# Kernel optimization log

Hardware: AMD Instinct MI355X
Metric: run time of the kernel (lower is better)

Reference implementation:

```python
import jax, jax.numpy as jnp
import numpy as np

# Dims: B=32 batch, C=64 feat channels, Np=192 priors, No=72 row offsets,
# Ns=36 pooled sample points (maxpool kernel 2), Hd=64 fc hidden.
B, C, Np, No, Hd = 32, 64, 192, 72, 64
NS_POOL = 2  # n_offsets // sample_points
REG_DIM = No + 4  # reg_layers output


def bilinear_sample(feat, gx, gy):
    """torch F.grid_sample(align_corners=True) equivalent for in-range coords.
    feat: [B,C,H,W]; gx,gy: [B,Np,S] normalized to [-1,1]. -> [B,C,Np,S]."""
    Bb, Cc, H, W = feat.shape
    ix = (gx + 1.0) * 0.5 * (W - 1)
    iy = (gy + 1.0) * 0.5 * (H - 1)
    ix0f = jnp.floor(ix); iy0f = jnp.floor(iy)
    wx = ix - ix0f; wy = iy - iy0f
    ix0 = jnp.clip(ix0f.astype(jnp.int32), 0, W - 1)
    iy0 = jnp.clip(iy0f.astype(jnp.int32), 0, H - 1)
    ix1 = jnp.clip(ix0 + 1, 0, W - 1)
    iy1 = jnp.clip(iy0 + 1, 0, H - 1)
    ff = feat.reshape(Bb, Cc, H * W)
    S = gx.shape[1] * gx.shape[2]
    def gather(iy_, ix_):
        idx = (iy_ * W + ix_).reshape(Bb, 1, S)
        g = jnp.take_along_axis(ff, jnp.broadcast_to(idx, (Bb, Cc, S)), axis=2)
        return g.reshape(Bb, Cc, gx.shape[1], gx.shape[2])
    v00 = gather(iy0, ix0); v01 = gather(iy0, ix1)
    v10 = gather(iy1, ix0); v11 = gather(iy1, ix1)
    wx = wx[:, None]; wy = wy[:, None]  # broadcast over C
    return (v00 * (1 - wx) * (1 - wy) + v01 * wx * (1 - wy)
            + v10 * (1 - wx) * wy + v11 * wx * wy)


def _mlp2(h, Ws, bs):
    # two stacked Linear+ReLU layers (num_fc=2)
    for i in range(2):
        h = jax.nn.relu(h @ Ws[i] + bs[i])
    return h


def setup_inputs() -> dict:
    key = jax.random.key(0)
    ks = jax.random.split(key, 24)
    w = lambda k, sh: jax.random.normal(k, sh, dtype=jnp.float32) * 0.05
    return {
        "x0": jax.random.normal(ks[0], (B, C, 40, 100), dtype=jnp.float32),
        "x1": jax.random.normal(ks[1], (B, C, 20, 50), dtype=jnp.float32),
        "x2": jax.random.normal(ks[2], (B, C, 10, 25), dtype=jnp.float32),
        "prior_xs0": jax.random.uniform(ks[3], (Np, No), dtype=jnp.float32),
        "l_weight": w(ks[4], (No,)),              # self.l embedding, sigmoid gate
        "lsgi_w": w(ks[5], (3, C, C)),            # per-stage lsgi projection
        "fc_w": w(ks[6], (C, Hd)), "fc_b": w(ks[7], (Hd,)),
        "cls_w": w(ks[8], (2, Hd, Hd)), "cls_b": w(ks[9], (2, Hd)),
        "cls_ow": w(ks[10], (Hd, 2)), "cls_ob": w(ks[11], (2,)),
        "reg_w": w(ks[12], (2, Hd, Hd)), "reg_b": w(ks[13], (2, Hd)),
        "reg_ow": w(ks[14], (Hd, REG_DIM)), "reg_ob": w(ks[15], (REG_DIM,)),
        "loc_w": w(ks[16], (2, Hd, Hd)), "loc_b": w(ks[17], (2, Hd)),
        "loc_ow": w(ks[18], (Hd, 1)), "loc_ob": w(ks[19], (1,)),
    }


def reference(x0, x1, x2, prior_xs0, l_weight, lsgi_w, fc_w, fc_b,
              cls_w, cls_b, cls_ow, cls_ob, reg_w, reg_b, reg_ow, reg_ob,
              loc_w, loc_b, loc_ow, loc_ob):
    pyramid = [x2, x1, x0]  # reversed: coarsest level first (stage 0)
    prior_feat_ys = jnp.linspace(1.0, 0.0, No, dtype=jnp.float32)
    gy = jnp.broadcast_to((prior_feat_ys * 2.0 - 1.0)[None, None, :], (B, Np, No))
    prior_xs = jnp.broadcast_to(prior_xs0[None], (B, Np, No))
    gate = jax.nn.sigmoid(l_weight)[:, None]  # [No,1]
    stage_feats = []
    outs = []
    for s in range(3):
        gx = prior_xs * 2.0 - 1.0
        pooled = bilinear_sample(pyramid[s], gx, gy)          # [B,C,Np,No]
        pooled = jnp.transpose(pooled, (0, 2, 3, 1)) * gate   # [B,Np,No,C]
        pooled = jax.nn.relu(jnp.einsum('bnoc,cd->bnod', pooled, lsgi_w[s]))
        # MaxPool2d kernel (2,1) over the offset axis -> Ns=36 sample points
        comp = pooled.reshape(B, Np, No // NS_POOL, NS_POOL, C).max(axis=3)
        stage_feats.append(comp)
        # cross-stage fusion (global head): mean over stages and sample points
        fused = jnp.stack(stage_feats, 0).mean(axis=0).mean(axis=2)  # [B,Np,C]
        fc = jax.nn.relu(fused @ fc_w + fc_b)                        # [B,Np,Hd]
        cls = _mlp2(fc, cls_w, cls_b) @ cls_ow + cls_ob              # [B,Np,2]
        reg = _mlp2(fc, reg_w, reg_b) @ reg_ow + reg_ob              # [B,Np,No+4]
        loc = _mlp2(fc, loc_w, loc_b) @ loc_ow + loc_ob              # [B,Np,1]
        outs.append(jnp.concatenate([cls, reg, loc], axis=-1))      # [B,Np,79]
        # refine anchors for next stage from predicted xs
        prior_xs = jax.nn.sigmoid(reg[..., 4:])
    return jnp.stack(outs, axis=0)  # [3,B,Np,79]
```

## Files before the change

### kernel.cpp

```cpp
#include <hip/hip_runtime.h>
#include <hip/hip_bf16.h>

#define Bq   32
#define Cq   64
#define NPq  192
#define NOq  72
#define PTS  (NPq * NOq)
#define REGD 76
#define OUTD 79

typedef __attribute__((ext_vector_type(8))) short short8;
typedef __attribute__((ext_vector_type(4))) float float4v;

__device__ inline unsigned short f2bf(float x) {
    __hip_bfloat16 h = __float2bfloat16(x);
    return *reinterpret_cast<unsigned short*>(&h);
}
__device__ inline float bf2f(unsigned short u) {
    unsigned int x = ((unsigned int)u) << 16;
    float f;
    __builtin_memcpy(&f, &x, 4);
    return f;
}

__global__ __launch_bounds__(256) void build_tables_kernel(
    const float* __restrict__ f0,
    const float* __restrict__ f1,
    const float* __restrict__ f2,
    const float* __restrict__ lw,
    unsigned short* __restrict__ t0,
    unsigned short* __restrict__ t1,
    unsigned short* __restrict__ t2)
{
    __shared__ float sRow[64 * 101];

    const int tid = threadIdx.x;
    const int o   = blockIdx.x / 96;
    const int sb  = blockIdx.x - o * 96;
    const int s   = sb >> 5;
    const int b   = sb & 31;

    const float* feat; unsigned short* tab; int H, W;
    if (s == 0)      { feat = f0; tab = t0; H = 10; W = 25; }
    else if (s == 1) { feat = f1; tab = t1; H = 20; W = 50; }
    else             { feat = f2; tab = t2; H = 40; W = 100; }
    const int Wp = W + 1;

    const float ys = 1.0f - (float)o * (1.0f / 71.0f);
    const float iy = ys * (float)(H - 1);
    const float fy = floorf(iy);
    const float wy = iy - fy;
    int iy0 = (int)fy; iy0 = iy0 < 0 ? 0 : (iy0 > H - 1 ? H - 1 : iy0);
    const int iy1 = (iy0 + 1 > H - 1) ? H - 1 : iy0 + 1;
    const float gate = 1.0f / (1.0f + __expf(-lw[o]));

    const float* fb = feat + (size_t)b * 64 * H * W;
    const int iy0W = iy0 * W, iy1W = iy1 * W;

    const int tot = 64 * W;
    for (int idx = tid; idx < tot; idx += 256) {
        const int c = idx / W;
        const int x = idx - c * W;
        const float* f = fb + c * (H * W);
        sRow[c * Wp + x] = ((1.0f - wy) * f[iy0W + x] + wy * f[iy1W + x]) * gate;
    }
    __syncthreads();

    unsigned short* to = tab + (size_t)(b * NOq + o) * Wp * 64;
    const int tot2 = Wp * 64;
    for (int idx = tid; idx < tot2; idx += 256) {
        const int x = idx >> 6;
        const int c = idx & 63;
        const int xx = (x < W) ? x : (W - 1);
        to[idx] = f2bf(sRow[c * Wp + xx]);
    }
}

template<int W>
__global__ __launch_bounds__(256) void fused_pool_head_kernel(
    const unsigned short* __restrict__ tab,
    const float* __restrict__ xsrc, const int xstride,
    const float* __restrict__ lsgi,
    float* __restrict__ sumFeat,
    const int stage,
    const float* __restrict__ fc_w,  const float* __restrict__ fc_b,
    const float* __restrict__ cls_w, const float* __restrict__ cls_b,
    const float* __restrict__ cls_ow, const float* __restrict__ cls_ob,
    const float* __restrict__ reg_w, const float* __restrict__ reg_b,
    const float* __restrict__ reg_ow, const float* __restrict__ reg_ob,
    const float* __restrict__ loc_w, const float* __restrict__ loc_b,
    const float* __restrict__ loc_ow, const float* __restrict__ loc_ob,
    float* __restrict__ out, float* __restrict__ xs_next)
{
    constexpr int Wp = W + 1;
    __shared__ __align__(16) float sF [8][68];
    __shared__ __align__(16) float sC [8][68];
    __shared__ __align__(16) float sT1[8][68];
    __shared__ __align__(16) float sT2[8][68];
    __shared__ __align__(16) float sWt[4864];

    const int tid  = threadIdx.x;
    const int w    = tid >> 6;
    const int lane = tid & 63;
    const int ng   = blockIdx.x >> 5;
    const int b    = blockIdx.x & 31;
    const int npair = ng * 4 + w;

    short8 wf[4][2];
    {
        const int kb = ((lane >> 4) & 3) * 8;
        const int dl = lane & 15;
        #pragma unroll
        for (int ks = 0; ks < 2; ++ks)
            #pragma unroll
            for (int dt = 0; dt < 4; ++dt) {
                union { unsigned short u[8]; short8 v; } pk;
                #pragma unroll
                for (int j = 0; j < 8; ++j)
                    pk.u[j] = f2bf(lsgi[(ks * 32 + kb + j) * 64 + dt * 16 + dl]);
                wf[dt][ks] = pk.v;
            }
    }

    const unsigned short* tb = tab + (size_t)b * NOq * Wp * 64;
    const float* xp = xsrc + (size_t)xstride * b;
    const int m  = lane & 15;
    const int kg = lane >> 4;
    const int nt0 = npair * 9;

    float sums0[4] = {0.f, 0.f, 0.f, 0.f};
    float sums1[4] = {0.f, 0.f, 0.f, 0.f};

    #pragma unroll
    for (int ntl = 0; ntl < 9; ++ntl) {
        const int pt = (nt0 + ntl) * 16 + m;
        const int o  = pt % NOq;
        float ixf = xp[pt] * (float)(W - 1);
        ixf = fminf(fmaxf(ixf, 0.0f), (float)(W - 1));
        const float fx = floorf(ixf);
        const float wx = ixf - fx;
        const int ix0 = (int)fx;

        const unsigned short* col = tb + ((size_t)o * Wp + ix0) * 64 + kg * 8;
        const short8 a00 = *(const short8*)(col);
        const short8 a01 = *(const short8*)(col + 64);
        const short8 a10 = *(const short8*)(col + 32);
        const short8 a11 = *(const short8*)(col + 96);

        float wxr[4];
        #pragma unroll
        for (int j = 0; j < 4; ++j) wxr[j] = __shfl(wx, kg * 4 + j);

        const bool hi = (ntl * 16 + (kg * 4)) >= NOq;
        #pragma unroll
        for (int dt = 0; dt < 4; ++dt) {
            float4v c0 = {0.f, 0.f, 0.f, 0.f};
            float4v c1 = {0.f, 0.f, 0.f, 0.f};
            c0 = __builtin_amdgcn_mfma_f32_16x16x32_bf16(a00, wf[dt][0], c0, 0, 0, 0);
            c0 = __builtin_amdgcn_mfma_f32_16x16x32_bf16(a10, wf[dt][1], c0, 0, 0, 0);
            c1 = __builtin_amdgcn_mfma_f32_16x16x32_bf16(a01, wf[dt][0], c1, 0, 0, 0);
            c1 = __builtin_amdgcn_mfma_f32_16x16x32_bf16(a11, wf[dt][1], c1, 0, 0, 0);
            const float v0 = c0[0] + wxr[0] * (c1[0] - c0[0]);
            const float v1 = c0[1] + wxr[1] * (c1[1] - c0[1]);
            const float v2 = c0[2] + wxr[2] * (c1[2] - c0[2]);
            const float v3 = c0[3] + wxr[3] * (c1[3] - c0[3]);
            const float pm0 = fmaxf(fmaxf(v0, v1), 0.f);
            const float pm1 = fmaxf(fmaxf(v2, v3), 0.f);
            const float add = pm0 + pm1;
            if (hi) sums1[dt] += add; else sums0[dt] += add;
        }
    }

    #pragma unroll
    for (int dt = 0; dt < 4; ++dt) {
        float v0 = sums0[dt], v1 = sums1[dt];
        v0 += __shfl_xor(v0, 16); v0 += __shfl_xor(v0, 32);
        v1 += __shfl_xor(v1, 16); v1 += __shfl_xor(v1, 32);
        sums0[dt] = v0; sums1[dt] = v1;
    }

    const float invS = 1.0f / (float)(stage + 1);
    if (lane < 16) {
        const size_t row0 = (size_t)(b * NPq + npair * 2) * 64;
        #pragma unroll
        for (int dt = 0; dt < 4; ++dt) {
            const int d = dt * 16 + lane;
            float t0 = sums0[dt] * (1.0f / 36.0f);
            float t1 = sums1[dt] * (1.0f / 36.0f);
            float* p0 = sumFeat + row0 + d;
            float* p1 = sumFeat + row0 + 64 + d;
            if (stage > 0) { t0 += *p0; t1 += *p1; }
            *p0 = t0; *p1 = t1;
            sF[2 * w][d]     = t0 * invS;
            sF[2 * w + 1][d] = t1 * invS;
        }
    }

    const int pt2 = tid >> 5;
    const int dh  = tid & 31;
    const int d0  = dh * 2;
    const int p0g = b * NPq + ng * 8;

    auto gemm64 = [&](const float (*src)[68], float (*dst)[68],
                      const float* __restrict__ gw, const float* __restrict__ gb) {
        __syncthreads();
        #pragma unroll
        for (int i = 0; i < 4; ++i)
            *(float4*)&sWt[(i * 256 + tid) * 4] = *(const float4*)&gw[(i * 256 + tid) * 4];
        __syncthreads();
        float a0 = gb[d0], a1 = gb[d0 + 1];
        #pragma unroll 8
        for (int k = 0; k < 64; ++k) {
            const float av = src[pt2][k];
            const float2 w2 = *(const float2*)&sWt[k * 64 + d0];
            a0 += av * w2.x; a1 += av * w2.y;
        }
        dst[pt2][d0]     = fmaxf(a0, 0.f);
        dst[pt2][d0 + 1] = fmaxf(a1, 0.f);
    };

    gemm64(sF, sC, fc_w, fc_b);

    gemm64(sC,  sT1, cls_w,        cls_b);
    gemm64(sT1, sT2, cls_w + 4096, cls_b + 64);
    __syncthreads();
    if (tid < 16) {
        const int p = tid >> 1, d = tid & 1;
        float z = cls_ob[d];
        #pragma unroll 8
        for (int k = 0; k < 64; ++k) z += sT2[p][k] * cls_ow[k * 2 + d];
        out[(size_t)(p0g + p) * OUTD + d] = z;
    }

    gemm64(sC,  sT1, reg_w,        reg_b);
    gemm64(sT1, sT2, reg_w + 4096, reg_b + 64);
    __syncthreads();
    for (int idx = tid; idx < 64 * REGD; idx += 256) sWt[idx] = reg_ow[idx];
    __syncthreads();
    {
        float* orow = out + (size_t)(p0g + pt2) * OUTD;
        float* xsp  = xs_next + (size_t)(p0g + pt2) * NOq;
        for (int j = dh; j < REGD; j += 32) {
            float z = reg_ob[j];
            #pragma unroll 8
            for (int k = 0; k < 64; ++k) z += sT2[pt2][k] * sWt[k * REGD + j];
            orow[2 + j] = z;
            if (j >= 4) xsp[j - 4] = 1.0f / (1.0f + __expf(-z));
        }
    }

    gemm64(sC,  sT1, loc_w,        loc_b);
    gemm64(sT1, sT2, loc_w + 4096, loc_b + 64);
    __syncthreads();
    if (tid < 8) {
        float z = loc_ob[0];
        #pragma unroll 8
        for (int k = 0; k < 64; ++k) z += sT2[tid][k] * loc_ow[k];
        out[(size_t)(p0g + tid) * OUTD + 78] = z;
    }
}

extern "C" void kernel_launch(void* const* d_in, const int* in_sizes, int n_in,
                              void* d_out, int out_size, void* d_ws, size_t ws_size,
                              hipStream_t stream)
{
    const float* x0        = (const float*)d_in[0];
    const float* x1        = (const float*)d_in[1];
    const float* x2        = (const float*)d_in[2];
    const float* prior_xs0 = (const float*)d_in[3];
    const float* l_weight  = (const float*)d_in[4];
    const float* lsgi_w    = (const float*)d_in[5];
    const float* fc_w      = (const float*)d_in[6];
    const float* fc_b      = (const float*)d_in[7];
    const float* cls_w     = (const float*)d_in[8];
    const float* cls_b     = (const float*)d_in[9];
    const float* cls_ow    = (const float*)d_in[10];
    const float* cls_ob    = (const float*)d_in[11];
    const float* reg_w     = (const float*)d_in[12];
    const float* reg_b     = (const float*)d_in[13];
    const float* reg_ow    = (const float*)d_in[14];
    const float* reg_ob    = (const float*)d_in[15];
    const float* loc_w     = (const float*)d_in[16];
    const float* loc_b     = (const float*)d_in[17];
    const float* loc_ow    = (const float*)d_in[18];
    const float* loc_ob    = (const float*)d_in[19];

    float* out     = (float*)d_out;
    float* sumFeat = (float*)d_ws;
    float* xs      = sumFeat + (size_t)Bq * NPq * Cq;
    unsigned short* tab0 = (unsigned short*)(xs + (size_t)Bq * PTS);
    unsigned short* tab1 = tab0 + (size_t)Bq * NOq * 26  * 64;
    unsigned short* tab2 = tab1 + (size_t)Bq * NOq * 51  * 64;

    hipLaunchKernelGGL(build_tables_kernel, dim3(3 * Bq * NOq), dim3(256), 0, stream,
                       x2, x1, x0, l_weight, tab0, tab1, tab2);

    for (int s = 0; s < 3; ++s) {
        const float* xsrc = (s == 0) ? prior_xs0 : xs;
        const int xstr    = (s == 0) ? 0 : PTS;
        const unsigned short* tb = (s == 0) ? tab0 : (s == 1) ? tab1 : tab2;
        float* outS = out + (size_t)s * Bq * NPq * OUTD;
        if (s == 0)
            hipLaunchKernelGGL((fused_pool_head_kernel<25>), dim3(Bq * 24), dim3(256), 0, stream,
                               tb, xsrc, xstr, lsgi_w + s * 4096, sumFeat, s,
                               fc_w, fc_b, cls_w, cls_b, cls_ow, cls_ob,
                               reg_w, reg_b, reg_ow, reg_ob,
                               loc_w, loc_b, loc_ow, loc_ob, outS, xs);
        else if (s == 1)
            hipLaunchKernelGGL((fused_pool_head_kernel<50>), dim3(Bq * 24), dim3(256), 0, stream,
                               tb, xsrc, xstr, lsgi_w + s * 4096, sumFeat, s,
                               fc_w, fc_b, cls_w, cls_b, cls_ow, cls_ob,
                               reg_w, reg_b, reg_ow, reg_ob,
                               loc_w, loc_b, loc_ow, loc_ob, outS, xs);
        else
            hipLaunchKernelGGL((fused_pool_head_kernel<100>), dim3(Bq * 24), dim3(256), 0, stream,
                               tb, xsrc, xstr, lsgi_w + s * 4096, sumFeat, s,
                               fc_w, fc_b, cls_w, cls_b, cls_ow, cls_ob,
                               reg_w, reg_b, reg_ow, reg_ob,
                               loc_w, loc_b, loc_ow, loc_ob, outS, xs);
    }
}
```

Baseline: 257.8 us.

## Fuse three per-stage pool/head kernels into one block-persistent kernel

```diff
diff --git a/kernel.cpp b/kernel.cpp
--- a/kernel.cpp
+++ b/kernel.cpp
@@ -15,12 +15,6 @@
 __device__ inline unsigned short f2bf(float x) {
     __hip_bfloat16 h = __float2bfloat16(x);
     return *reinterpret_cast<unsigned short*>(&h);
-}
-__device__ inline float bf2f(unsigned short u) {
-    unsigned int x = ((unsigned int)u) << 16;
-    float f;
-    __builtin_memcpy(&f, &x, 4);
-    return f;
 }
 
 __global__ __launch_bounds__(256) void build_tables_kernel(
@@ -76,13 +70,13 @@
     }
 }
 
-template<int W>
-__global__ __launch_bounds__(256) void fused_pool_head_kernel(
+template<int W, int STAGE>
+__device__ __forceinline__ void pool_head_stage(
+    float (*sF)[68], float (*sC)[68], float (*sT1)[68], float (*sT2)[68],
+    float* sWt, float (*sXs)[72], float (*sSum)[64],
     const unsigned short* __restrict__ tab,
-    const float* __restrict__ xsrc, const int xstride,
+    const float* __restrict__ prior0,
     const float* __restrict__ lsgi,
-    float* __restrict__ sumFeat,
-    const int stage,
     const float* __restrict__ fc_w,  const float* __restrict__ fc_b,
     const float* __restrict__ cls_w, const float* __restrict__ cls_b,
     const float* __restrict__ cls_ow, const float* __restrict__ cls_ob,
@@ -90,14 +84,9 @@
     const float* __restrict__ reg_ow, const float* __restrict__ reg_ob,
     const float* __restrict__ loc_w, const float* __restrict__ loc_b,
     const float* __restrict__ loc_ow, const float* __restrict__ loc_ob,
-    float* __restrict__ out, float* __restrict__ xs_next)
+    float* out)
 {
     constexpr int Wp = W + 1;
-    __shared__ __align__(16) float sF [8][68];
-    __shared__ __align__(16) float sC [8][68];
-    __shared__ __align__(16) float sT1[8][68];
-    __shared__ __align__(16) float sT2[8][68];
-    __shared__ __align__(16) float sWt[4864];
 
     const int tid  = threadIdx.x;
     const int w    = tid >> 6;
@@ -123,19 +112,23 @@
     }
 
     const unsigned short* tb = tab + (size_t)b * NOq * Wp * 64;
-    const float* xp = xsrc + (size_t)xstride * b;
     const int m  = lane & 15;
     const int kg = lane >> 4;
-    const int nt0 = npair * 9;
 
     float sums0[4] = {0.f, 0.f, 0.f, 0.f};
     float sums1[4] = {0.f, 0.f, 0.f, 0.f};
 
     #pragma unroll
     for (int ntl = 0; ntl < 9; ++ntl) {
-        const int pt = (nt0 + ntl) * 16 + m;
-        const int o  = pt % NOq;
-        float ixf = xp[pt] * (float)(W - 1);
+        const int ptl = (w * 9 + ntl) * 16 + m;
+        const int o   = ptl % NOq;
+        float xval;
+        if (STAGE == 0) {
+            xval = prior0[npair * 144 + ntl * 16 + m];
+        } else {
+            xval = sXs[ptl / NOq][o];
+        }
+        float ixf = xval * (float)(W - 1);
         ixf = fminf(fmaxf(ixf, 0.0f), (float)(W - 1));
         const float fx = floorf(ixf);
         const float wx = ixf - fx;
@@ -179,18 +172,16 @@
         sums0[dt] = v0; sums1[dt] = v1;
     }
 
-    const float invS = 1.0f / (float)(stage + 1);
+    constexpr float invS = 1.0f / (float)(STAGE + 1);
     if (lane < 16) {
-        const size_t row0 = (size_t)(b * NPq + npair * 2) * 64;
         #pragma unroll
         for (int dt = 0; dt < 4; ++dt) {
             const int d = dt * 16 + lane;
             float t0 = sums0[dt] * (1.0f / 36.0f);
             float t1 = sums1[dt] * (1.0f / 36.0f);
-            float* p0 = sumFeat + row0 + d;
-            float* p1 = sumFeat + row0 + 64 + d;
-            if (stage > 0) { t0 += *p0; t1 += *p1; }
-            *p0 = t0; *p1 = t1;
+            if (STAGE > 0) { t0 += sSum[2 * w][d]; t1 += sSum[2 * w + 1][d]; }
+            sSum[2 * w][d]     = t0;
+            sSum[2 * w + 1][d] = t1;
             sF[2 * w][d]     = t0 * invS;
             sF[2 * w + 1][d] = t1 * invS;
         }
@@ -239,13 +230,12 @@
     __syncthreads();
     {
         float* orow = out + (size_t)(p0g + pt2) * OUTD;
-        float* xsp  = xs_next + (size_t)(p0g + pt2) * NOq;
         for (int j = dh; j < REGD; j += 32) {
             float z = reg_ob[j];
             #pragma unroll 8
             for (int k = 0; k < 64; ++k) z += sT2[pt2][k] * sWt[k * REGD + j];
             orow[2 + j] = z;
-            if (j >= 4) xsp[j - 4] = 1.0f / (1.0f + __expf(-z));
+            if (j >= 4) sXs[pt2][j - 4] = 1.0f / (1.0f + __expf(-z));
         }
     }
 
@@ -258,6 +248,48 @@
         for (int k = 0; k < 64; ++k) z += sT2[tid][k] * loc_ow[k];
         out[(size_t)(p0g + tid) * OUTD + 78] = z;
     }
+}
+
+__global__ __launch_bounds__(256) void fused3_kernel(
+    const unsigned short* __restrict__ tab0,
+    const unsigned short* __restrict__ tab1,
+    const unsigned short* __restrict__ tab2,
+    const float* __restrict__ prior_xs0, const float* __restrict__ lsgi_w,
+    const float* __restrict__ fc_w,  const float* __restrict__ fc_b,
+    const float* __restrict__ cls_w, const float* __restrict__ cls_b,
+    const float* __restrict__ cls_ow, const float* __restrict__ cls_ob,
+    const float* __restrict__ reg_w, const float* __restrict__ reg_b,
+    const float* __restrict__ reg_ow, const float* __restrict__ reg_ob,
+    const float* __restrict__ loc_w, const float* __restrict__ loc_b,
+    const float* __restrict__ loc_ow, const float* __restrict__ loc_ob,
+    float* out)
+{
+    __shared__ __align__(16) float sF [8][68];
+    __shared__ __align__(16) float sC [8][68];
+    __shared__ __align__(16) float sT1[8][68];
+    __shared__ __align__(16) float sT2[8][68];
+    __shared__ __align__(16) float sWt[4864];
+    __shared__ __align__(16) float sXs[8][72];
+    __shared__ __align__(16) float sSum[8][64];
+
+    pool_head_stage<25, 0>(sF, sC, sT1, sT2, sWt, sXs, sSum, tab0, prior_xs0,
+                           lsgi_w,
+                           fc_w, fc_b, cls_w, cls_b, cls_ow, cls_ob,
+                           reg_w, reg_b, reg_ow, reg_ob,
+                           loc_w, loc_b, loc_ow, loc_ob,
+                           out);
+    pool_head_stage<50, 1>(sF, sC, sT1, sT2, sWt, sXs, sSum, tab1, nullptr,
+                           lsgi_w + 4096,
+                           fc_w, fc_b, cls_w, cls_b, cls_ow, cls_ob,
+                           reg_w, reg_b, reg_ow, reg_ob,
+                           loc_w, loc_b, loc_ow, loc_ob,
+                           out + (size_t)Bq * NPq * OUTD);
+    pool_head_stage<100, 2>(sF, sC, sT1, sT2, sWt, sXs, sSum, tab2, nullptr,
+                            lsgi_w + 8192,
+                            fc_w, fc_b, cls_w, cls_b, cls_ow, cls_ob,
+                            reg_w, reg_b, reg_ow, reg_ob,
+                            loc_w, loc_b, loc_ow, loc_ob,
+                            out + (size_t)2 * Bq * NPq * OUTD);
 }
 
 extern "C" void kernel_launch(void* const* d_in, const int* in_sizes, int n_in,
@@ -285,38 +317,17 @@
     const float* loc_ow    = (const float*)d_in[18];
     const float* loc_ob    = (const float*)d_in[19];
 
-    float* out     = (float*)d_out;
-    float* sumFeat = (float*)d_ws;
-    float* xs      = sumFeat + (size_t)Bq * NPq * Cq;
-    unsigned short* tab0 = (unsigned short*)(xs + (size_t)Bq * PTS);
+    float* out = (float*)d_out;
+    unsigned short* tab0 = (unsigned short*)d_ws;
     unsigned short* tab1 = tab0 + (size_t)Bq * NOq * 26  * 64;
     unsigned short* tab2 = tab1 + (size_t)Bq * NOq * 51  * 64;
 
     hipLaunchKernelGGL(build_tables_kernel, dim3(3 * Bq * NOq), dim3(256), 0, stream,
                        x2, x1, x0, l_weight, tab0, tab1, tab2);
 
-    for (int s = 0; s < 3; ++s) {
-        const float* xsrc = (s == 0) ? prior_xs0 : xs;
-        const int xstr    = (s == 0) ? 0 : PTS;
-        const unsigned short* tb = (s == 0) ? tab0 : (s == 1) ? tab1 : tab2;
-        float* outS = out + (size_t)s * Bq * NPq * OUTD;
-        if (s == 0)
-            hipLaunchKernelGGL((fused_pool_head_kernel<25>), dim3(Bq * 24), dim3(256), 0, stream,
-                               tb, xsrc, xstr, lsgi_w + s * 4096, sumFeat, s,
-                               fc_w, fc_b, cls_w, cls_b, cls_ow, cls_ob,
-                               reg_w, reg_b, reg_ow, reg_ob,
-                               loc_w, loc_b, loc_ow, loc_ob, outS, xs);
-        else if (s == 1)
-            hipLaunchKernelGGL((fused_pool_head_kernel<50>), dim3(Bq * 24), dim3(256), 0, stream,
-                               tb, xsrc, xstr, lsgi_w + s * 4096, sumFeat, s,
-                               fc_w, fc_b, cls_w, cls_b, cls_ow, cls_ob,
-                               reg_w, reg_b, reg_ow, reg_ob,
-                               loc_w, loc_b, loc_ow, loc_ob, outS, xs);
-        else
-            hipLaunchKernelGGL((fused_pool_head_kernel<100>), dim3(Bq * 24), dim3(256), 0, stream,
-                               tb, xsrc, xstr, lsgi_w + s * 4096, sumFeat, s,
-                               fc_w, fc_b, cls_w, cls_b, cls_ow, cls_ob,
-                               reg_w, reg_b, reg_ow, reg_ob,
-                               loc_w, loc_b, loc_ow, loc_ob, outS, xs);
-    }
-}
+    hipLaunchKernelGGL(fused3_kernel, dim3(Bq * 24), dim3(256), 0, stream,
+                       tab0, tab1, tab2, prior_xs0, lsgi_w,
+                       fc_w, fc_b, cls_w, cls_b, cls_ow, cls_ob,
+                       reg_w, reg_b, reg_ow, reg_ob,
+                       loc_w, loc_b, loc_ow, loc_ob, out);
+}
```

New measurement: 317.7 us. +23.2%, slower.
